# Kernel optimization log

Measured on AMD Instinct MI355X. Metric: run time of the kernel, lower is better.

## Reference

```python
import jax, jax.numpy as jnp
import numpy as np

H, W = 512, 512          # image_shape
FH, FW = 64, 64          # filter_size
NUM_PARTS = 256
N = 8192                 # number of placed parts


def setup_inputs() -> dict:
    key = jax.random.key(0)
    k1, k2, k3, k4 = jax.random.split(key, 4)
    filters = jax.random.normal(k1, (NUM_PARTS, FH, FW), dtype=jnp.float32)
    part = jax.random.randint(k2, (N,), 0, NUM_PARTS)
    row = jax.random.randint(k3, (N,), 0, H)
    col = jax.random.randint(k4, (N,), 0, W)
    phw_list = jnp.stack([part, row, col], axis=1).astype(jnp.int32)  # [N,3]
    return {"phw_list": phw_list, "filters": filters}


def reference(phw_list, filters):
    # Original: for each part i, slice filters[part_idx] to the in-bounds window
    # and += into canvas[from_r:to_r, from_c:to_c].
    # Equivalent vectorized form: scatter-add FULL filters onto a padded canvas
    # (pad = full filter size on each side, so all writes are in-bounds), then
    # crop back to (H, W). Clipping via crop == the original's slice clipping.
    fo_h, fo_w = FH // 2, FW // 2  # filter center offsets
    part = phw_list[:, 0]
    row = phw_list[:, 1]
    col = phw_list[:, 2]

    filts = filters[part]                                  # (N, FH, FW) gather
    r0 = row - fo_h + FH                                   # top-left row in padded canvas
    c0 = col - fo_w + FW                                   # top-left col in padded canvas
    rr = r0[:, None, None] + jnp.arange(FH)[None, :, None]  # (N, FH, 1)
    cc = c0[:, None, None] + jnp.arange(FW)[None, None, :]  # (N, 1, FW)

    padded = jnp.zeros((H + 2 * FH, W + 2 * FW), dtype=filters.dtype)
    padded = padded.at[rr, cc].add(filts)                  # overlapping scatter-add
    return padded[FH:FH + H, FW:FW + W]                    # (H, W) canvas
```

## Files before the change

### kernel.cpp

```cpp
#include <hip/hip_runtime.h>


#define H_  512
#define W_  512
#define FH_ 64
#define FW_ 64
#define TILE_ 32
#define SEG_LEN_ 1024

__global__ __launch_bounds__(256)
void render_tile_kernel(const int* __restrict__ phw,
                        const float* __restrict__ filters,
                        float* __restrict__ out, int n) {
    __shared__ unsigned int s_list[SEG_LEN_];
    __shared__ int s_cnt;

    const int t   = threadIdx.x;
    const int tx0 = blockIdx.x * TILE_;
    const int ty0 = blockIdx.y * TILE_;
    const int k0  = blockIdx.z * SEG_LEN_;
    const int k1  = (k0 + SEG_LEN_ < n) ? (k0 + SEG_LEN_) : n;

    if (t == 0) s_cnt = 0;
    __syncthreads();

    for (int k = k0 + t; k < k1; k += 256) {
        const int part = phw[k * 3 + 0];
        const int row  = phw[k * 3 + 1];
        const int col  = phw[k * 3 + 2];
        const bool hit =
            (row >= ty0 - (FH_ / 2 - 1)) && (row <= ty0 + TILE_ - 1 + FH_ / 2) &&
            (col >= tx0 - (FW_ / 2 - 1)) && (col <= tx0 + TILE_ - 1 + FW_ / 2);
        if (hit) {
            const int idx = atomicAdd(&s_cnt, 1);
            s_list[idx] = ((unsigned)part << 18) | ((unsigned)row << 9) | (unsigned)col;
        }
    }
    __syncthreads();
    const int cnt = s_cnt;

    const int xl = t & 31;
    const int yb = t >> 5;
    const int x  = tx0 + xl;

    float acc0 = 0.f, acc1 = 0.f, acc2 = 0.f, acc3 = 0.f;

#pragma unroll 2
    for (int k = 0; k < cnt; ++k) {
        const unsigned v = s_list[k];
        const int part = (int)(v >> 18);
        const int row  = (int)((v >> 9) & 511u);
        const int col  = (int)(v & 511u);

        const int j = x - col + (FW_ / 2);
        if ((unsigned)j < (unsigned)FW_) {
            const float* f = filters + part * (FH_ * FW_) + j;
            const int i0 = ty0 + yb - row + (FH_ / 2);
            int i;
            i = i0;      if ((unsigned)i < (unsigned)FH_) acc0 += f[i * FW_];
            i = i0 + 8;  if ((unsigned)i < (unsigned)FH_) acc1 += f[i * FW_];
            i = i0 + 16; if ((unsigned)i < (unsigned)FH_) acc2 += f[i * FW_];
            i = i0 + 24; if ((unsigned)i < (unsigned)FH_) acc3 += f[i * FW_];
        }
    }

    const int yo = ty0 + yb;
    atomicAdd(&out[(yo +  0) * W_ + x], acc0);
    atomicAdd(&out[(yo +  8) * W_ + x], acc1);
    atomicAdd(&out[(yo + 16) * W_ + x], acc2);
    atomicAdd(&out[(yo + 24) * W_ + x], acc3);
}

extern "C" void kernel_launch(void* const* d_in, const int* in_sizes, int n_in,
                              void* d_out, int out_size, void* d_ws, size_t ws_size,
                              hipStream_t stream) {
    const int*   phw     = (const int*)d_in[0];
    const float* filters = (const float*)d_in[1];
    float*       out     = (float*)d_out;
    const int n = in_sizes[0] / 3;

    hipMemsetAsync(out, 0, (size_t)H_ * W_ * sizeof(float), stream);

    const int segs = (n + SEG_LEN_ - 1) / SEG_LEN_;
    dim3 grid(W_ / TILE_, H_ / TILE_, segs);
    render_tile_kernel<<<grid, 256, 0, stream>>>(phw, filters, out, n);
}
```

Baseline: 101.7 us.

## Use 128-thread blocks with 8 contiguous rows per thread and shorter segments

Blocks shrink from 256 to 128 threads. Each thread now accumulates 8 consecutive rows of its column instead of 4 strided rows, and the part list is split into segments of 512 instead of 1024, which doubles the z-dimension of the grid. Each filter reference now yields more accumulations per thread, and the extra blocks raise parallelism. The cost is more per-block list filtering work relative to the total and twice as many global atomic flushes to the output canvas.

```diff
diff --git a/kernel.cpp b/kernel.cpp
--- a/kernel.cpp
+++ b/kernel.cpp
@@ -6,9 +6,10 @@
 #define FH_ 64
 #define FW_ 64
 #define TILE_ 32
-#define SEG_LEN_ 1024
+#define THREADS_ 128
+#define SEG_LEN_ 512
 
-__global__ __launch_bounds__(256)
+__global__ __launch_bounds__(THREADS_, 8)
 void render_tile_kernel(const int* __restrict__ phw,
                         const float* __restrict__ filters,
                         float* __restrict__ out, int n) {
@@ -24,7 +25,7 @@
     if (t == 0) s_cnt = 0;
     __syncthreads();
 
-    for (int k = k0 + t; k < k1; k += 256) {
+    for (int k = k0 + t; k < k1; k += THREADS_) {
         const int part = phw[k * 3 + 0];
         const int row  = phw[k * 3 + 1];
         const int col  = phw[k * 3 + 2];
@@ -39,11 +40,12 @@
     __syncthreads();
     const int cnt = s_cnt;
 
-    const int xl = t & 31;
-    const int yb = t >> 5;
-    const int x  = tx0 + xl;
+    const int xl    = t & 31;
+    const int yb    = t >> 5;
+    const int x     = tx0 + xl;
+    const int ybase = ty0 + yb * 8;
 
-    float acc0 = 0.f, acc1 = 0.f, acc2 = 0.f, acc3 = 0.f;
+    float acc[8] = {0.f, 0.f, 0.f, 0.f, 0.f, 0.f, 0.f, 0.f};
 
 #pragma unroll 2
     for (int k = 0; k < cnt; ++k) {
@@ -55,20 +57,19 @@
         const int j = x - col + (FW_ / 2);
         if ((unsigned)j < (unsigned)FW_) {
             const float* f = filters + part * (FH_ * FW_) + j;
-            const int i0 = ty0 + yb - row + (FH_ / 2);
-            int i;
-            i = i0;      if ((unsigned)i < (unsigned)FH_) acc0 += f[i * FW_];
-            i = i0 + 8;  if ((unsigned)i < (unsigned)FH_) acc1 += f[i * FW_];
-            i = i0 + 16; if ((unsigned)i < (unsigned)FH_) acc2 += f[i * FW_];
-            i = i0 + 24; if ((unsigned)i < (unsigned)FH_) acc3 += f[i * FW_];
+            const int i0 = ybase - row + (FH_ / 2);
+#pragma unroll
+            for (int q = 0; q < 8; ++q) {
+                const int i = i0 + q;
+                if ((unsigned)i < (unsigned)FH_) acc[q] += f[i * FW_];
+            }
         }
     }
 
-    const int yo = ty0 + yb;
-    atomicAdd(&out[(yo +  0) * W_ + x], acc0);
-    atomicAdd(&out[(yo +  8) * W_ + x], acc1);
-    atomicAdd(&out[(yo + 16) * W_ + x], acc2);
-    atomicAdd(&out[(yo + 24) * W_ + x], acc3);
+#pragma unroll
+    for (int q = 0; q < 8; ++q) {
+        atomicAdd(&out[(ybase + q) * W_ + x], acc[q]);
+    }
 }
 
 extern "C" void kernel_launch(void* const* d_in, const int* in_sizes, int n_in,
@@ -83,5 +84,5 @@
 
     const int segs = (n + SEG_LEN_ - 1) / SEG_LEN_;
     dim3 grid(W_ / TILE_, H_ / TILE_, segs);
-    render_tile_kernel<<<grid, 256, 0, stream>>>(phw, filters, out, n);
+    render_tile_kernel<<<grid, THREADS_, 0, stream>>>(phw, filters, out, n);
 }
```

New measurement: 109.2 us. 7.4% more time.
